# Performance work log

Measured on AMD Instinct MI355X. Metric: run time of the kernel, lower is better.

Reference implementation:

```python
import jax, jax.numpy as jnp
import numpy as np

B, LT, D, H, DI = 8, 128, 512, 8, 2048
NMEM, LMEM = 1024, 64
DH = D // H
EPS = 1e-5
NEG = -1e9

def _ln(x, g, b):
    mu = x.mean(-1, keepdims=True)
    var = ((x - mu) ** 2).mean(-1, keepdims=True)
    return (x - mu) * jax.lax.rsqrt(var + EPS) * g + b

def _ffn(x, W1, b1, W2, b2):
    # PositionwiseFF with residual=True (dropout=0 / eval)
    return x + jax.nn.relu(x @ W1 + b1) @ W2 + b2

def setup_inputs():
    key = jax.random.key(0)
    ks = jax.random.split(key, 16)
    w = lambda i, shape: jax.random.normal(ks[i], shape, jnp.float32) * 0.02
    return {
        "dec_output": jax.random.normal(ks[0], (B, LT, D), jnp.float32),
        "mem_attn_out": jax.random.normal(ks[1], (B, LT, NMEM + 1), jnp.float32),
        "enc_out_mem": jax.random.normal(ks[2], (NMEM, LMEM, D), jnp.float32),
        "tgt_emb_mem": jax.random.normal(ks[3], (NMEM, LMEM, D), jnp.float32),
        "tgt_mask_mem": jax.random.randint(ks[4], (NMEM, LMEM), 0, 2, jnp.int32),
        "tgt_mask": jax.random.randint(ks[5], (B, LT), 0, 2, jnp.int32),
        "g0": jnp.ones((D,), jnp.float32), "be0": jnp.zeros((D,), jnp.float32),
        "g1": jnp.ones((D,), jnp.float32), "be1": jnp.zeros((D,), jnp.float32),
        "Wq": w(6, (D, D)), "bq": jnp.zeros((D,), jnp.float32),
        "Wk": w(7, (D, D)), "bk": jnp.zeros((D,), jnp.float32),
        "Wv": w(8, (D, D)), "bv": jnp.zeros((D,), jnp.float32),
        "Wo": w(9, (D, D)), "bo": jnp.zeros((D,), jnp.float32),
        "f1W1": w(10, (D, DI)), "f1b1": jnp.zeros((DI,), jnp.float32),
        "f1W2": w(11, (DI, D)), "f1b2": jnp.zeros((D,), jnp.float32),
        "f2W1": w(12, (D, DI)), "f2b1": jnp.zeros((DI,), jnp.float32),
        "f2W2": w(13, (DI, D)), "f2b2": jnp.zeros((D,), jnp.float32),
    }

def reference(dec_output, mem_attn_out, enc_out_mem, tgt_emb_mem, tgt_mask_mem, tgt_mask,
              g0, be0, g1, be1, Wq, bq, Wk, bk, Wv, bv, Wo, bo,
              f1W1, f1b1, f1W2, f1b2, f2W1, f2b1, f2W2, f2b2):
    x = _ln(dec_output, g0, be0)                       # [B,LT,D]
    N = B * LT
    samples = jnp.argmax(mem_attn_out, -1).reshape(N) - 1   # [-1, NMEM-1]
    valid = samples >= 0                               # [N]
    s = jnp.maximum(samples, 0)                        # clamp; masked later
    q = x.reshape(N, 1, D)
    # gather memory per selected query (torch compacts via unique; same math)
    k_in = enc_out_mem[s]                              # [N,LMEM,D]
    v_in = tgt_emb_mem[s]                              # [N,LMEM,D]
    kmask = tgt_mask_mem[s] != 0                       # True = valid key
    # multi-head attention, residual=True
    qh = (q @ Wq + bq).reshape(N, 1, H, DH).transpose(0, 2, 1, 3)     # [N,H,1,DH]
    kh = (k_in @ Wk + bk).reshape(N, LMEM, H, DH).transpose(0, 2, 1, 3)
    vh = (v_in @ Wv + bv).reshape(N, LMEM, H, DH).transpose(0, 2, 1, 3)
    scores = jnp.einsum('nhqd,nhkd->nhqk', qh, kh) / (DH ** 0.5)      # [N,H,1,LMEM]
    scores = jnp.where(kmask[:, None, None, :], scores, NEG)
    attn = jax.nn.softmax(scores, axis=-1)
    ctx = jnp.einsum('nhqk,nhkd->nhqd', attn, vh).transpose(0, 2, 1, 3).reshape(N, 1, D)
    st = q + ctx @ Wo + bo
    st = _ffn(st, f1W1, f1b1, f1W2, f1b2)
    st = _ln(st, g1, be1)
    # scatter back: positions with sample == -1 get zeros
    st = jnp.where(valid[:, None, None], st, 0.0)
    dec = x + st.reshape(B, LT, D)
    dec = _ffn(dec, f2W1, f2b1, f2W2, f2b2)
    return dec
```

## Files before the change

kernel.cpp:

```cpp
#include <hip/hip_runtime.h>
#include <math.h>

#define NQ   1024
#define DIM  512
#define NH   8
#define DHD  64
#define DFF  2048
#define LM   64

typedef __bf16 bf16x8 __attribute__((ext_vector_type(8)));
typedef float  f32x4  __attribute__((ext_vector_type(4)));

__device__ __forceinline__ unsigned short f2bf(float f) {
    unsigned u = __builtin_bit_cast(unsigned, f);
    return (unsigned short)((u + 0x7fffu + ((u >> 16) & 1u)) >> 16);
}
__device__ __forceinline__ float bflo(unsigned p) {
    return __builtin_bit_cast(float, p << 16);
}
__device__ __forceinline__ float bfhi(unsigned p) {
    return __builtin_bit_cast(float, p & 0xffff0000u);
}

__device__ __forceinline__ void gload16(const void* g, void* l) {
    __builtin_amdgcn_global_load_lds(
        (const __attribute__((address_space(1))) unsigned*)g,
        (__attribute__((address_space(3))) unsigned*)l, 16, 0, 0);
}

__device__ __forceinline__ float blk_sum(float v, volatile float* red) {
#pragma unroll
    for (int o = 32; o; o >>= 1) v += __shfl_down(v, o);
    __syncthreads();
    if ((threadIdx.x & 63) == 0) red[threadIdx.x >> 6] = v;
    __syncthreads();
    return red[0] + red[1] + red[2] + red[3];
}

struct PrepPtrs {
    const float* src[8];
    unsigned short* dst[8];
};
__global__ __launch_bounds__(256) void prep_ln0_k(
    PrepPtrs p,
    const float* __restrict__ dec_out, const float* __restrict__ attn_out,
    const float* __restrict__ g, const float* __restrict__ be,
    float* __restrict__ x, unsigned* __restrict__ xb, int* __restrict__ samples)
{
    __shared__ float tile[32][33];
    __shared__ float red[4];
    __shared__ float rv[4]; __shared__ int ri[4];
    const int bid = blockIdx.x;

    if (bid < 5120) {
        int m, lt;
        if (bid < 1024) { m = bid >> 8; lt = bid & 255; }
        else { m = 4 + ((bid - 1024) >> 10); lt = (bid - 1024) & 1023; }
        const int RS = (m < 4) ? 512 : ((m == 5 || m == 7) ? 2048 : 512);
        const int CS = (m < 4) ? 512 : ((m == 5 || m == 7) ? 512 : 2048);
        const int TC = CS >> 5;
        const int tr = lt / TC, tc = lt % TC;
        const float* s = p.src[m];
        unsigned short* d = p.dst[m];
        const int tx = threadIdx.x & 31, ty = threadIdx.x >> 5;
        if (m == 1) {
#pragma unroll
            for (int i = 0; i < 32; i += 8) {
                size_t idx = (size_t)(tr * 32 + ty + i) * CS + tc * 32 + tx;
                d[idx] = f2bf(s[idx]);
            }
        } else {
#pragma unroll
            for (int i = 0; i < 32; i += 8)
                tile[ty + i][tx] = s[(size_t)(tr * 32 + ty + i) * CS + tc * 32 + tx];
            __syncthreads();
#pragma unroll
            for (int i = 0; i < 32; i += 8)
                d[(size_t)(tc * 32 + ty + i) * RS + tr * 32 + tx] = f2bf(tile[tx][ty + i]);
        }
        return;
    }

    const int n = bid - 5120, t = threadIdx.x;
    float2 v = ((const float2*)(dec_out + (size_t)n * DIM))[t];
    float mu  = blk_sum(v.x + v.y, red) * (1.f / DIM);
    float dx = v.x - mu, dy = v.y - mu;
    float var = blk_sum(dx * dx + dy * dy, red) * (1.f / DIM);
    float rs = rsqrtf(var + 1e-5f);
    float2 gg = ((const float2*)g)[t], bb = ((const float2*)be)[t];
    float ox = dx * rs * gg.x + bb.x, oy = dy * rs * gg.y + bb.y;
    ((float2*)(x + (size_t)n * DIM))[t] = make_float2(ox, oy);
    xb[(size_t)n * 256 + t] = (unsigned)f2bf(ox) | ((unsigned)f2bf(oy) << 16);

    const float* ar = attn_out + (size_t)n * 1025;
    float bv = -INFINITY; int bi = 0x7fffffff;
    for (int i = t; i < 1025; i += 256) {
        float val = ar[i];
        if (val > bv || (val == bv && i < bi)) { bv = val; bi = i; }
    }
#pragma unroll
    for (int o = 32; o; o >>= 1) {
        float ov = __shfl_down(bv, o); int oi = __shfl_down(bi, o);
        if (ov > bv || (ov == bv && oi < bi)) { bv = ov; bi = oi; }
    }
    if ((t & 63) == 0) { rv[t >> 6] = bv; ri[t >> 6] = bi; }
    __syncthreads();
    if (t == 0) {
#pragma unroll
        for (int w = 1; w < 4; ++w)
            if (rv[w] > bv || (rv[w] == bv && ri[w] < bi)) { bv = rv[w]; bi = ri[w]; }
        samples[n] = bi - 1;
    }
}

template<bool RELU, bool BIAS, bool RES, bool WF32, bool WBF>
__global__ __launch_bounds__(256) void mfma_gemm(
    const unsigned short* __restrict__ A, const unsigned short* __restrict__ Bt,
    float* __restrict__ Cf, unsigned short* __restrict__ Cb,
    const float* __restrict__ bias, const float* __restrict__ res,
    int K, int lda, int ldb, int ldc,
    int sA, int sB, int sC, int sBias)
{
    __shared__ unsigned short Ab[2][64 * 64];
    __shared__ unsigned short Bb[2][64 * 64];
    const int t = threadIdx.x, lane = t & 63, wid = t >> 6;
    const int nx = gridDim.x;
    const int fid = blockIdx.y * nx + blockIdx.x;
    const int cpx = (nx * gridDim.y) >> 3;
    const int f2 = (fid & 7) * cpx + (fid >> 3);
    const int bn = (f2 % nx) * 64, bm = (f2 / nx) * 64, bz = blockIdx.z;
    const unsigned short* Abase = A + (size_t)bz * sA + (size_t)bm * lda;
    const unsigned short* Bbase = Bt + (size_t)bz * sB + (size_t)bn * ldb;

    const int r0 = wid * 16 + (lane >> 3);
    const int cbs = lane & 7;

#define STAGE_T(buf, base, ld, kt)                                              \
    {                                                                           \
        int r_ = r0;                                                            \
        gload16(base + (size_t)r_ * ld + (kt) * 64 + ((cbs ^ (r_ & 7)) << 3),   \
                &buf[(wid * 2 + 0) * 512]);                                     \
        r_ = r0 + 8;                                                            \
        gload16(base + (size_t)r_ * ld + (kt) * 64 + ((cbs ^ (r_ & 7)) << 3),   \
                &buf[(wid * 2 + 1) * 512]);                                     \
    }

    const int lr = lane & 15, lg = lane >> 4;
    const int wr = (wid >> 1) * 32, wc = (wid & 1) * 32;
    const int mA0 = wr + lr, mA1 = wr + 16 + lr;
    const int nB0 = wc + lr, nB1 = wc + 16 + lr;
    f32x4 acc[2][2] = {};

#define COMPUTE(b)                                                              \
    _Pragma("unroll")                                                           \
    for (int kk = 0; kk < 2; ++kk) {                                            \
        const int kb = kk * 4 + lg;                                             \
        bf16x8 a0 = *(const bf16x8*)&Ab[b][mA0 * 64 + ((kb ^ (mA0 & 7)) << 3)]; \
        bf16x8 a1 = *(const bf16x8*)&Ab[b][mA1 * 64 + ((kb ^ (mA1 & 7)) << 3)]; \
        bf16x8 b0 = *(const bf16x8*)&Bb[b][nB0 * 64 + ((kb ^ (nB0 & 7)) << 3)]; \
        bf16x8 b1 = *(const bf16x8*)&Bb[b][nB1 * 64 + ((kb ^ (nB1 & 7)) << 3)]; \
        acc[0][0] = __builtin_amdgcn_mfma_f32_16x16x32_bf16(a0, b0, acc[0][0], 0, 0, 0); \
        acc[0][1] = __builtin_amdgcn_mfma_f32_16x16x32_bf16(a0, b1, acc[0][1], 0, 0, 0); \
        acc[1][0] = __builtin_amdgcn_mfma_f32_16x16x32_bf16(a1, b0, acc[1][0], 0, 0, 0); \
        acc[1][1] = __builtin_amdgcn_mfma_f32_16x16x32_bf16(a1, b1, acc[1][1], 0, 0, 0); \
    }

    STAGE_T(Ab[0], Abase, lda, 0);
    STAGE_T(Bb[0], Bbase, ldb, 0);
    __syncthreads();
    const int NT = K >> 6;
    int cur = 0;
    for (int kt = 0; kt < NT; ++kt) {
        if (kt + 1 < NT) {
            STAGE_T(Ab[cur ^ 1], Abase, lda, kt + 1);
            STAGE_T(Bb[cur ^ 1], Bbase, ldb, kt + 1);
        }
        if (cur == 0) { COMPUTE(0); } else { COMPUTE(1); }
        __syncthreads();
        cur ^= 1;
    }

#pragma unroll
    for (int fm = 0; fm < 2; ++fm)
#pragma unroll
    for (int fn = 0; fn < 2; ++fn) {
        const int col = bn + wc + fn * 16 + lr;
        float bia = BIAS ? bias[bz * sBias + col] : 0.f;
#pragma unroll
        for (int r = 0; r < 4; ++r) {
            const int row = bm + wr + fm * 16 + lg * 4 + r;
            const size_t ci = (size_t)bz * sC + (size_t)row * ldc + col;
            float v = acc[fm][fn][r] + bia;
            if (RES) v += res[(size_t)row * ldc + col];
            if (RELU) v = fmaxf(v, 0.f);
            if (WF32) Cf[ci] = v;
            if (WBF)  Cb[ci] = f2bf(v);
        }
    }
#undef STAGE_T
#undef COMPUTE
}

__global__ __launch_bounds__(256) void attn_scores_k(
    const unsigned short* __restrict__ u_bf, const float* __restrict__ enc,
    const int* __restrict__ samples, float* __restrict__ s_part)
{
    const int n = blockIdx.x, q = blockIdx.y, t = threadIdx.x;
    const int lane = t & 63, w = t >> 6;
    int s = samples[n]; if (s < 0) s = 0;

    const float4* kb = (const float4*)(enc + (size_t)s * (LM * DIM));
    const int key = w * 16 + (lane & 15);
    const int lg = lane >> 4;
    const int h = lane & 15;
    const int base = key * 128 + q * 32 + lg * 2;
    float4 pf[4][2];
#pragma unroll
    for (int ss = 0; ss < 4; ++ss) {
        pf[ss][0] = kb[base + ss * 8];
        pf[ss][1] = kb[base + ss * 8 + 1];
    }

    const unsigned short* ub = u_bf + (size_t)n * 4096 + (size_t)(h & 7) * 512 + q * 128;
    f32x4 acc = {};
#pragma unroll
    for (int step = 0; step < 4; ++step) {
        float4 a0 = pf[step][0], a1 = pf[step][1];
        bf16x8 af;
        af[0] = (__bf16)a0.x; af[1] = (__bf16)a0.y;
        af[2] = (__bf16)a0.z; af[3] = (__bf16)a0.w;
        af[4] = (__bf16)a1.x; af[5] = (__bf16)a1.y;
        af[6] = (__bf16)a1.z; af[7] = (__bf16)a1.w;
        bf16x8 bfr = *(const bf16x8*)&ub[(step * 4 + lg) * 8];
        acc = __builtin_amdgcn_mfma_f32_16x16x32_bf16(af, bfr, acc, 0, 0, 0);
    }
    if (h < 8) {
        float* sp = s_part + (((size_t)n * 4 + q) * 8 + h) * 64 + w * 16 + lg * 4;
        *(float4*)sp = make_float4(acc[0], acc[1], acc[2], acc[3]);
    }
}

__global__ __launch_bounds__(256) void attn_pv_k(
    const float* __restrict__ s_part, const float* __restrict__ vemb,
    const int* __restrict__ maskmem, const int* __restrict__ samples,
    unsigned* __restrict__ a_bf)
{
    __shared__ float Sp_lds[2048];
    __shared__ uint4 P_lds[64];
    __shared__ float2 Red[3][8][64];
    __shared__ int Msk_lds[64];
    const int n = blockIdx.x, dq = blockIdx.y, t = threadIdx.x;
    const int lane = t & 63, w = t >> 6;
    int s = samples[n]; if (s < 0) s = 0;

    ((float4*)Sp_lds)[t]       = ((const float4*)(s_part + (size_t)n * 2048))[t];
    ((float4*)Sp_lds)[t + 256] = ((const float4*)(s_part + (size_t)n * 2048))[t + 256];
    if (t < 64) Msk_lds[t] = maskmem[(size_t)s * LM + t];
    __syncthreads();

#pragma unroll
    for (int hh = 0; hh < 2; ++hh) {
        const int h = w + hh * 4;
        float sc = (Sp_lds[h * 64 + lane] + Sp_lds[512 + h * 64 + lane]
                  + Sp_lds[1024 + h * 64 + lane] + Sp_lds[1536 + h * 64 + lane]) * 0.125f;
        sc = (Msk_lds[lane] != 0) ? sc : -1e9f;
        float m = sc;
#pragma unroll
        for (int o = 32; o; o >>= 1) m = fmaxf(m, __shfl_xor(m, o));
        float e = __expf(sc - m);
        float su = e;
#pragma unroll
        for (int o = 32; o; o >>= 1) su += __shfl_xor(su, o);
        ((unsigned short*)P_lds)[lane * 8 + h] = f2bf(e / su);
    }
    __syncthreads();

    const int c = t & 63, kh = t >> 6;
    const float2* vb = (const float2*)(vemb + (size_t)s * (LM * DIM)) + dq * 64 + c;
    float2 acc8[8];
#pragma unroll
    for (int hh = 0; hh < 8; ++hh) acc8[hh] = make_float2(0.f, 0.f);
#pragma unroll 8
    for (int i = 0; i < 16; ++i) {
        const int k = kh * 16 + i;
        float2 v = vb[(size_t)k * 256];
        uint4 pr = P_lds[k];
        float p0 = bflo(pr.x), p1 = bfhi(pr.x);
        float p2 = bflo(pr.y), p3 = bfhi(pr.y);
        float p4 = bflo(pr.z), p5 = bfhi(pr.z);
        float p6 = bflo(pr.w), p7 = bfhi(pr.w);
        acc8[0].x = fmaf(p0, v.x, acc8[0].x); acc8[0].y = fmaf(p0, v.y, acc8[0].y);
        acc8[1].x = fmaf(p1, v.x, acc8[1].x); acc8[1].y = fmaf(p1, v.y, acc8[1].y);
        acc8[2].x = fmaf(p2, v.x, acc8[2].x); acc8[2].y = fmaf(p2, v.y, acc8[2].y);
        acc8[3].x = fmaf(p3, v.x, acc8[3].x); acc8[3].y = fmaf(p3, v.y, acc8[3].y);
        acc8[4].x = fmaf(p4, v.x, acc8[4].x); acc8[4].y = fmaf(p4, v.y, acc8[4].y);
        acc8[5].x = fmaf(p5, v.x, acc8[5].x); acc8[5].y = fmaf(p5, v.y, acc8[5].y);
        acc8[6].x = fmaf(p6, v.x, acc8[6].x); acc8[6].y = fmaf(p6, v.y, acc8[6].y);
        acc8[7].x = fmaf(p7, v.x, acc8[7].x); acc8[7].y = fmaf(p7, v.y, acc8[7].y);
    }
    if (kh > 0) {
#pragma unroll
        for (int hh = 0; hh < 8; ++hh) Red[kh - 1][hh][c] = acc8[hh];
    }
    __syncthreads();
    if (kh == 0) {
        unsigned* an = a_bf + (size_t)n * 2048 + dq * 64;
#pragma unroll
        for (int hh = 0; hh < 8; ++hh) {
            float2 r0 = Red[0][hh][c], r1 = Red[1][hh][c], r2 = Red[2][hh][c];
            float ox = acc8[hh].x + r0.x + r1.x + r2.x;
            float oy = acc8[hh].y + r0.y + r1.y + r2.y;
            an[hh * 256 + c] = (unsigned)f2bf(ox) | ((unsigned)f2bf(oy) << 16);
        }
    }
}

__global__ __launch_bounds__(256) void ln1_mask_add_k(
    const float* __restrict__ t1p, const float* __restrict__ st0,
    const float* __restrict__ b2, const float* __restrict__ g,
    const float* __restrict__ be, const int* __restrict__ samples,
    const float* __restrict__ x, float* __restrict__ dec, unsigned* __restrict__ decb)
{
    __shared__ float red[4];
    const int n = blockIdx.x, t = threadIdx.x;
    const size_t off = (size_t)n * DIM + t * 2;
    float2 p0 = *(const float2*)&t1p[off];
    float2 p1 = *(const float2*)&t1p[(size_t)NQ * DIM + off];
    float2 s0 = *(const float2*)&st0[off];
    float2 b2v = ((const float2*)b2)[t];
    float2 v = make_float2(p0.x + p1.x + s0.x + b2v.x, p0.y + p1.y + s0.y + b2v.y);
    float mu  = blk_sum(v.x + v.y, red) * (1.f / DIM);
    float dx = v.x - mu, dy = v.y - mu;
    float var = blk_sum(dx * dx + dy * dy, red) * (1.f / DIM);
    float rs = rsqrtf(var + 1e-5f);
    float2 gg = ((const float2*)g)[t], bb = ((const float2*)be)[t];
    float sx = dx * rs * gg.x + bb.x, sy = dy * rs * gg.y + bb.y;
    if (samples[n] < 0) { sx = 0.f; sy = 0.f; }
    float2 xx = *(const float2*)&x[off];
    float ox = xx.x + sx, oy = xx.y + sy;
    *(float2*)&dec[off] = make_float2(ox, oy);
    decb[(size_t)n * 256 + t] = (unsigned)f2bf(ox) | ((unsigned)f2bf(oy) << 16);
}

extern "C" void kernel_launch(void* const* d_in, const int* in_sizes, int n_in,
                              void* d_out, int out_size, void* d_ws, size_t ws_size,
                              hipStream_t stream)
{
    const float* dec_output = (const float*)d_in[0];
    const float* mem_attn   = (const float*)d_in[1];
    const float* enc_mem    = (const float*)d_in[2];
    const float* temb_mem   = (const float*)d_in[3];
    const int*   mask_mem   = (const int*)d_in[4];
    const float* g0  = (const float*)d_in[6];
    const float* be0 = (const float*)d_in[7];
    const float* g1  = (const float*)d_in[8];
    const float* be1 = (const float*)d_in[9];
    const float* Wq  = (const float*)d_in[10];
    const float* bq  = (const float*)d_in[11];
    const float* Wk  = (const float*)d_in[12];
    const float* Wv  = (const float*)d_in[14];
    const float* bv  = (const float*)d_in[15];
    const float* Wo  = (const float*)d_in[16];
    const float* bo  = (const float*)d_in[17];
    const float* f1W1 = (const float*)d_in[18];
    const float* f1b1 = (const float*)d_in[19];
    const float* f1W2 = (const float*)d_in[20];
    const float* f1b2 = (const float*)d_in[21];
    const float* f2W1 = (const float*)d_in[22];
    const float* f2b1 = (const float*)d_in[23];
    const float* f2W2 = (const float*)d_in[24];
    const float* f2b2 = (const float*)d_in[25];
    float* out = (float*)d_out;

    float* ws = (float*)d_ws;
    float*          x_f   = ws + 0;
    unsigned*       x_b   = (unsigned*)(ws + 524288);
    unsigned short* qh_b  = (unsigned short*)(ws + 786432);
    unsigned short* u_b   = (unsigned short*)(ws + 1048576);
    unsigned short* a_b   = (unsigned short*)(ws + 3145728);
    float*          s_prt = ws + 5242880;
    unsigned short* wqt   = (unsigned short*)(ws + 7340032);
    unsigned short* wkc   = (unsigned short*)(ws + 7471104);
    unsigned short* wvt   = (unsigned short*)(ws + 7602176);
    unsigned short* wot   = (unsigned short*)(ws + 7733248);
    unsigned short* f1w1t = (unsigned short*)(ws + 7864320);
    unsigned short* f1w2t = (unsigned short*)(ws + 8388608);
    unsigned short* f2w1t = (unsigned short*)(ws + 8912896);
    unsigned short* f2w2t = (unsigned short*)(ws + 9437184);
    int*            smp   = (int*)(ws + 9961472);
    float*          t1p_f = ws + 9962496;
    float*          st0_f = (float*)u_b + 0;
    unsigned short* st0_b = (unsigned short*)((float*)u_b + 524288);
    float*          dec_f = (float*)u_b + 655360;
    unsigned*       dec_b = (unsigned*)((float*)u_b + 1179648);
    unsigned short* h1_b  = a_b;
    unsigned short* h2_b  = (unsigned short*)((float*)a_b + 1048576);

    PrepPtrs pp;
    pp.src[0] = Wq;   pp.dst[0] = wqt;
    pp.src[1] = Wk;   pp.dst[1] = wkc;
    pp.src[2] = Wv;   pp.dst[2] = wvt;
    pp.src[3] = Wo;   pp.dst[3] = wot;
    pp.src[4] = f1W1; pp.dst[4] = f1w1t;
    pp.src[5] = f1W2; pp.dst[5] = f1w2t;
    pp.src[6] = f2W1; pp.dst[6] = f2w1t;
    pp.src[7] = f2W2; pp.dst[7] = f2w2t;
    prep_ln0_k<<<5120 + NQ, 256, 0, stream>>>(pp, dec_output, mem_attn, g0, be0,
                                              x_f, x_b, smp);
    mfma_gemm<false, true, false, false, true><<<dim3(8, 16, 1), 256, 0, stream>>>(
        (const unsigned short*)x_b, wqt, nullptr, qh_b, bq, nullptr,
        DIM, DIM, DIM, DIM, 0, 0, 0, 0);
    mfma_gemm<false, false, false, false, true><<<dim3(8, 16, NH), 256, 0, stream>>>(
        qh_b, wkc, nullptr, u_b, nullptr, nullptr,
        DHD, DIM, DIM, NH * DIM, DHD, DHD, DIM, 0);
    attn_scores_k<<<dim3(NQ, 4), 256, 0, stream>>>(u_b, enc_mem, smp, s_prt);
    attn_pv_k<<<dim3(NQ, 4), 256, 0, stream>>>(s_prt, temb_mem, mask_mem, smp,
                                               (unsigned*)a_b);
    mfma_gemm<false, true, false, false, true><<<dim3(1, 16, NH), 256, 0, stream>>>(
        a_b, wvt, nullptr, qh_b, bv, nullptr,
        DIM, NH * DIM, DIM, DIM, DIM, DHD * DIM, DHD, DHD);
    mfma_gemm<false, true, true, true, true><<<dim3(8, 16, 1), 256, 0, stream>>>(
        qh_b, wot, st0_f, st0_b, bo, x_f, DIM, DIM, DIM, DIM, 0, 0, 0, 0);
    mfma_gemm<true, true, false, false, true><<<dim3(32, 16, 1), 256, 0, stream>>>(
        st0_b, f1w1t, nullptr, h1_b, f1b1, nullptr, DIM, DIM, DIM, DFF, 0, 0, 0, 0);
    mfma_gemm<false, false, false, true, false><<<dim3(8, 16, 2), 256, 0, stream>>>(
        h1_b, f1w2t, t1p_f, nullptr, nullptr, nullptr,
        1024, DFF, DFF, DIM, 1024, 1024, NQ * DIM, 0);
    ln1_mask_add_k<<<NQ, 256, 0, stream>>>(t1p_f, st0_f, f1b2, g1, be1, smp,
                                           x_f, dec_f, dec_b);
    mfma_gemm<true, true, false, false, true><<<dim3(32, 16, 1), 256, 0, stream>>>(
        (const unsigned short*)dec_b, f2w1t, nullptr, h2_b, f2b1, nullptr,
        DIM, DIM, DIM, DFF, 0, 0, 0, 0);
    mfma_gemm<false, true, true, true, false><<<dim3(8, 16, 1), 256, 0, stream>>>(
        h2_b, f2w2t, out, nullptr, f2b2, dec_f, DFF, DFF, DFF, DIM, 0, 0, 0, 0);

    (void)in_sizes; (void)n_in; (void)out_size; (void)ws_size;
}
```

Before: 156.7 us.

## Fuse partial softmax into score kernel and split keys across blocks

The score kernel now splits work by key halves instead of D-quarters. Each block reduces the full 512-dim dot product in-block through LDS, applies the mask, and computes a local softmax (max, sum, unnormalized bf16 exp). The PV kernel then merges the two halves with flash-style rescaling instead of re-reading 2048 float partial scores per query and redoing the softmax. The change also software-pipelines the K loads, reorders the PV grid so the four D-quarter blocks of one query are adjacent, and cuts intermediate traffic. The cost is an extra bf16 rounding of the rescaled probabilities and fewer, heavier score blocks.

Result: faster. 153.2 us (-2.2%).

```diff
diff --git a/kernel.cpp b/kernel.cpp
--- a/kernel.cpp
+++ b/kernel.cpp
@@ -203,29 +203,36 @@
 
 __global__ __launch_bounds__(256) void attn_scores_k(
     const unsigned short* __restrict__ u_bf, const float* __restrict__ enc,
-    const int* __restrict__ samples, float* __restrict__ s_part)
-{
-    const int n = blockIdx.x, q = blockIdx.y, t = threadIdx.x;
+    const int* __restrict__ maskmem, const int* __restrict__ samples,
+    unsigned short* __restrict__ p_half, float* __restrict__ msc)
+{
+    __shared__ float S_lds[2][32][8];
+    const int n = blockIdx.x, kq = blockIdx.y, t = threadIdx.x;
     const int lane = t & 63, w = t >> 6;
     int s = samples[n]; if (s < 0) s = 0;
 
-    const float4* kb = (const float4*)(enc + (size_t)s * (LM * DIM));
-    const int key = w * 16 + (lane & 15);
+    const int keyloc = (w & 1) * 16 + (lane & 15);
+    const int key = kq * 32 + keyloc;
+    const int dh = w >> 1;
     const int lg = lane >> 4;
     const int h = lane & 15;
-    const int base = key * 128 + q * 32 + lg * 2;
+    const float4* kb = (const float4*)(enc + (size_t)s * (LM * DIM));
+    const int base = key * 128 + dh * 64 + lg * 2;
     float4 pf[4][2];
 #pragma unroll
     for (int ss = 0; ss < 4; ++ss) {
         pf[ss][0] = kb[base + ss * 8];
         pf[ss][1] = kb[base + ss * 8 + 1];
     }
-
-    const unsigned short* ub = u_bf + (size_t)n * 4096 + (size_t)(h & 7) * 512 + q * 128;
+    const unsigned short* ub = u_bf + (size_t)n * 4096 + (size_t)(h & 7) * 512 + dh * 256;
     f32x4 acc = {};
 #pragma unroll
-    for (int step = 0; step < 4; ++step) {
-        float4 a0 = pf[step][0], a1 = pf[step][1];
+    for (int step = 0; step < 8; ++step) {
+        float4 a0 = pf[step & 3][0], a1 = pf[step & 3][1];
+        if (step + 4 < 8) {
+            pf[step & 3][0] = kb[base + (step + 4) * 8];
+            pf[step & 3][1] = kb[base + (step + 4) * 8 + 1];
+        }
         bf16x8 af;
         af[0] = (__bf16)a0.x; af[1] = (__bf16)a0.y;
         af[2] = (__bf16)a0.z; af[3] = (__bf16)a0.w;
@@ -235,43 +242,54 @@
         acc = __builtin_amdgcn_mfma_f32_16x16x32_bf16(af, bfr, acc, 0, 0, 0);
     }
     if (h < 8) {
-        float* sp = s_part + (((size_t)n * 4 + q) * 8 + h) * 64 + w * 16 + lg * 4;
-        *(float4*)sp = make_float4(acc[0], acc[1], acc[2], acc[3]);
-    }
+#pragma unroll
+        for (int r = 0; r < 4; ++r)
+            S_lds[dh][(w & 1) * 16 + lg * 4 + r][h] = acc[r];
+    }
+    __syncthreads();
+
+    const int h2 = t >> 5, k2 = t & 31;
+    float sc = (S_lds[0][k2][h2] + S_lds[1][k2][h2]) * 0.125f;
+    const int mk = maskmem[(size_t)s * LM + kq * 32 + k2];
+    sc = (mk != 0) ? sc : -1e9f;
+    float m = sc;
+#pragma unroll
+    for (int o = 16; o; o >>= 1) m = fmaxf(m, __shfl_xor(m, o));
+    float e = __expf(sc - m);
+    float su = e;
+#pragma unroll
+    for (int o = 16; o; o >>= 1) su += __shfl_xor(su, o);
+    p_half[((size_t)n * 2 + kq) * 256 + k2 * 8 + h2] = f2bf(e);
+    if (k2 == 0)
+        ((float2*)(msc + ((size_t)n * 2 + kq) * 16))[h2] = make_float2(m, su);
 }
 
 __global__ __launch_bounds__(256) void attn_pv_k(
-    const float* __restrict__ s_part, const float* __restrict__ vemb,
-    const int* __restrict__ maskmem, const int* __restrict__ samples,
+    const unsigned short* __restrict__ p_half, const float* __restrict__ msc,
+    const float* __restrict__ vemb, const int* __restrict__ samples,
     unsigned* __restrict__ a_bf)
 {
-    __shared__ float Sp_lds[2048];
     __shared__ uint4 P_lds[64];
     __shared__ float2 Red[3][8][64];
-    __shared__ int Msk_lds[64];
-    const int n = blockIdx.x, dq = blockIdx.y, t = threadIdx.x;
-    const int lane = t & 63, w = t >> 6;
+    __shared__ float Wh[2][8];
+    const int dq = blockIdx.x, n = blockIdx.y, t = threadIdx.x;
     int s = samples[n]; if (s < 0) s = 0;
 
-    ((float4*)Sp_lds)[t]       = ((const float4*)(s_part + (size_t)n * 2048))[t];
-    ((float4*)Sp_lds)[t + 256] = ((const float4*)(s_part + (size_t)n * 2048))[t + 256];
-    if (t < 64) Msk_lds[t] = maskmem[(size_t)s * LM + t];
-    __syncthreads();
-
-#pragma unroll
-    for (int hh = 0; hh < 2; ++hh) {
-        const int h = w + hh * 4;
-        float sc = (Sp_lds[h * 64 + lane] + Sp_lds[512 + h * 64 + lane]
-                  + Sp_lds[1024 + h * 64 + lane] + Sp_lds[1536 + h * 64 + lane]) * 0.125f;
-        sc = (Msk_lds[lane] != 0) ? sc : -1e9f;
-        float m = sc;
-#pragma unroll
-        for (int o = 32; o; o >>= 1) m = fmaxf(m, __shfl_xor(m, o));
-        float e = __expf(sc - m);
-        float su = e;
-#pragma unroll
-        for (int o = 32; o; o >>= 1) su += __shfl_xor(su, o);
-        ((unsigned short*)P_lds)[lane * 8 + h] = f2bf(e / su);
+    if (t < 8) {
+        float2 ms0 = ((const float2*)(msc + (size_t)n * 32))[t];
+        float2 ms1 = ((const float2*)(msc + (size_t)n * 32 + 16))[t];
+        float m = fmaxf(ms0.x, ms1.x);
+        float w0 = __expf(ms0.x - m), w1 = __expf(ms1.x - m);
+        float inv = 1.f / (ms0.y * w0 + ms1.y * w1);
+        Wh[0][t] = w0 * inv; Wh[1][t] = w1 * inv;
+    }
+    __syncthreads();
+    {
+        const int k = t >> 2, hp = t & 3, kq = k >> 5;
+        unsigned v = ((const unsigned*)p_half)[((size_t)n * 2 + kq) * 128 + (k & 31) * 4 + hp];
+        float a = bflo(v) * Wh[kq][hp * 2];
+        float b = bfhi(v) * Wh[kq][hp * 2 + 1];
+        ((unsigned*)P_lds)[k * 4 + hp] = (unsigned)f2bf(a) | ((unsigned)f2bf(b) << 16);
     }
     __syncthreads();
 
@@ -378,7 +396,8 @@
     unsigned short* qh_b  = (unsigned short*)(ws + 786432);
     unsigned short* u_b   = (unsigned short*)(ws + 1048576);
     unsigned short* a_b   = (unsigned short*)(ws + 3145728);
-    float*          s_prt = ws + 5242880;
+    unsigned short* p_hlf = (unsigned short*)(ws + 5242880);
+    float*          msc   = ws + 5505024;
     unsigned short* wqt   = (unsigned short*)(ws + 7340032);
     unsigned short* wkc   = (unsigned short*)(ws + 7471104);
     unsigned short* wvt   = (unsigned short*)(ws + 7602176);
@@ -413,8 +432,9 @@
     mfma_gemm<false, false, false, false, true><<<dim3(8, 16, NH), 256, 0, stream>>>(
         qh_b, wkc, nullptr, u_b, nullptr, nullptr,
         DHD, DIM, DIM, NH * DIM, DHD, DHD, DIM, 0);
-    attn_scores_k<<<dim3(NQ, 4), 256, 0, stream>>>(u_b, enc_mem, smp, s_prt);
-    attn_pv_k<<<dim3(NQ, 4), 256, 0, stream>>>(s_prt, temb_mem, mask_mem, smp,
+    attn_scores_k<<<dim3(NQ, 2), 256, 0, stream>>>(u_b, enc_mem, mask_mem, smp,
+                                                   p_hlf, msc);
+    attn_pv_k<<<dim3(4, NQ), 256, 0, stream>>>(p_hlf, msc, temb_mem, smp,
                                                (unsigned*)a_b);
     mfma_gemm<false, true, false, false, true><<<dim3(1, 16, NH), 256, 0, stream>>>(
         a_b, wvt, nullptr, qh_b, bv, nullptr,
```

## Fuse attention scores, softmax and PV into one warp-specialized kernel

Applied to the files above, without the earlier changes.

Merges the separate score and PV kernels into one 512-thread block per query. Four waves compute the full QK scores over all of D with register-prefetched MFMA, while the other four waves prefetch V rows in parallel, then do the whole 64-key PV loop themselves. This drops the global score-partial round trip, one launch, and the cross-wave LDS reduction. The cost is fewer, larger blocks and longer serial loops per thread, which may reduce parallelism and occupancy.

New measurement: 149.9 us. 1.05x faster.

```diff
diff --git a/kernel.cpp b/kernel.cpp
--- a/kernel.cpp
+++ b/kernel.cpp
@@ -201,117 +201,106 @@
 #undef COMPUTE
 }
 
-__global__ __launch_bounds__(256) void attn_scores_k(
+__global__ __launch_bounds__(512) void attn_fused_k(
     const unsigned short* __restrict__ u_bf, const float* __restrict__ enc,
-    const int* __restrict__ samples, float* __restrict__ s_part)
+    const float* __restrict__ vemb, const int* __restrict__ maskmem,
+    const int* __restrict__ samples, unsigned* __restrict__ a_bf)
 {
-    const int n = blockIdx.x, q = blockIdx.y, t = threadIdx.x;
+    __shared__ float S_lds[8 * 68];
+    __shared__ uint4 P_lds[64];
+    __shared__ int Msk_lds[64];
+    const int n = blockIdx.x, t = threadIdx.x;
     const int lane = t & 63, w = t >> 6;
     int s = samples[n]; if (s < 0) s = 0;
 
-    const float4* kb = (const float4*)(enc + (size_t)s * (LM * DIM));
-    const int key = w * 16 + (lane & 15);
-    const int lg = lane >> 4;
-    const int h = lane & 15;
-    const int base = key * 128 + q * 32 + lg * 2;
-    float4 pf[4][2];
-#pragma unroll
-    for (int ss = 0; ss < 4; ++ss) {
-        pf[ss][0] = kb[base + ss * 8];
-        pf[ss][1] = kb[base + ss * 8 + 1];
-    }
-
-    const unsigned short* ub = u_bf + (size_t)n * 4096 + (size_t)(h & 7) * 512 + q * 128;
-    f32x4 acc = {};
-#pragma unroll
-    for (int step = 0; step < 4; ++step) {
-        float4 a0 = pf[step][0], a1 = pf[step][1];
-        bf16x8 af;
-        af[0] = (__bf16)a0.x; af[1] = (__bf16)a0.y;
-        af[2] = (__bf16)a0.z; af[3] = (__bf16)a0.w;
-        af[4] = (__bf16)a1.x; af[5] = (__bf16)a1.y;
-        af[6] = (__bf16)a1.z; af[7] = (__bf16)a1.w;
-        bf16x8 bfr = *(const bf16x8*)&ub[(step * 4 + lg) * 8];
-        acc = __builtin_amdgcn_mfma_f32_16x16x32_bf16(af, bfr, acc, 0, 0, 0);
-    }
-    if (h < 8) {
-        float* sp = s_part + (((size_t)n * 4 + q) * 8 + h) * 64 + w * 16 + lg * 4;
-        *(float4*)sp = make_float4(acc[0], acc[1], acc[2], acc[3]);
-    }
-}
-
-__global__ __launch_bounds__(256) void attn_pv_k(
-    const float* __restrict__ s_part, const float* __restrict__ vemb,
-    const int* __restrict__ maskmem, const int* __restrict__ samples,
-    unsigned* __restrict__ a_bf)
-{
-    __shared__ float Sp_lds[2048];
-    __shared__ uint4 P_lds[64];
-    __shared__ float2 Red[3][8][64];
-    __shared__ int Msk_lds[64];
-    const int n = blockIdx.x, dq = blockIdx.y, t = threadIdx.x;
-    const int lane = t & 63, w = t >> 6;
-    int s = samples[n]; if (s < 0) s = 0;
-
-    ((float4*)Sp_lds)[t]       = ((const float4*)(s_part + (size_t)n * 2048))[t];
-    ((float4*)Sp_lds)[t + 256] = ((const float4*)(s_part + (size_t)n * 2048))[t + 256];
-    if (t < 64) Msk_lds[t] = maskmem[(size_t)s * LM + t];
-    __syncthreads();
-
-#pragma unroll
-    for (int hh = 0; hh < 2; ++hh) {
-        const int h = w + hh * 4;
-        float sc = (Sp_lds[h * 64 + lane] + Sp_lds[512 + h * 64 + lane]
-                  + Sp_lds[1024 + h * 64 + lane] + Sp_lds[1536 + h * 64 + lane]) * 0.125f;
-        sc = (Msk_lds[lane] != 0) ? sc : -1e9f;
-        float m = sc;
-#pragma unroll
-        for (int o = 32; o; o >>= 1) m = fmaxf(m, __shfl_xor(m, o));
-        float e = __expf(sc - m);
-        float su = e;
-#pragma unroll
-        for (int o = 32; o; o >>= 1) su += __shfl_xor(su, o);
-        ((unsigned short*)P_lds)[lane * 8 + h] = f2bf(e / su);
-    }
-    __syncthreads();
-
-    const int c = t & 63, kh = t >> 6;
-    const float2* vb = (const float2*)(vemb + (size_t)s * (LM * DIM)) + dq * 64 + c;
-    float2 acc8[8];
-#pragma unroll
-    for (int hh = 0; hh < 8; ++hh) acc8[hh] = make_float2(0.f, 0.f);
+    float2 pfv[8];
+    const float2* vb = (const float2*)(vemb + (size_t)s * (LM * DIM)) + (t - 256);
+
+    if (w >= 4) {
+#pragma unroll
+        for (int i = 0; i < 8; ++i) pfv[i] = vb[(size_t)i * 256];
+        if (w == 4) Msk_lds[lane] = maskmem[(size_t)s * LM + lane];
+    } else {
+        const float4* kb = (const float4*)(enc + (size_t)s * (LM * DIM));
+        const int key = w * 16 + (lane & 15);
+        const int lg = lane >> 4;
+        const int h = lane & 15;
+        const int base = key * 128 + lg * 2;
+        float4 pf[4][2];
+#pragma unroll
+        for (int ss = 0; ss < 4; ++ss) {
+            pf[ss][0] = kb[base + ss * 8];
+            pf[ss][1] = kb[base + ss * 8 + 1];
+        }
+        const unsigned short* ub = u_bf + (size_t)n * 4096 + (size_t)(h & 7) * 512;
+        f32x4 acc = {};
+#pragma unroll
+        for (int step = 0; step < 16; ++step) {
+            float4 a0 = pf[step & 3][0], a1 = pf[step & 3][1];
+            if (step + 4 < 16) {
+                pf[step & 3][0] = kb[base + (step + 4) * 8];
+                pf[step & 3][1] = kb[base + (step + 4) * 8 + 1];
+            }
+            bf16x8 af;
+            af[0] = (__bf16)a0.x; af[1] = (__bf16)a0.y;
+            af[2] = (__bf16)a0.z; af[3] = (__bf16)a0.w;
+            af[4] = (__bf16)a1.x; af[5] = (__bf16)a1.y;
+            af[6] = (__bf16)a1.z; af[7] = (__bf16)a1.w;
+            bf16x8 bfr = *(const bf16x8*)&ub[(step * 4 + lg) * 8];
+            acc = __builtin_amdgcn_mfma_f32_16x16x32_bf16(af, bfr, acc, 0, 0, 0);
+        }
+        if (h < 8) {
+#pragma unroll
+            for (int r = 0; r < 4; ++r)
+                S_lds[h * 68 + w * 16 + lg * 4 + r] = acc[r];
+        }
+    }
+    __syncthreads();
+
+    if (w < 4) {
+#pragma unroll
+        for (int hh = 0; hh < 2; ++hh) {
+            const int h2 = w + hh * 4;
+            float sc = S_lds[h2 * 68 + lane] * 0.125f;
+            sc = (Msk_lds[lane] != 0) ? sc : -1e9f;
+            float m = sc;
+#pragma unroll
+            for (int o = 32; o; o >>= 1) m = fmaxf(m, __shfl_xor(m, o));
+            float e = __expf(sc - m);
+            float su = e;
+#pragma unroll
+            for (int o = 32; o; o >>= 1) su += __shfl_xor(su, o);
+            ((unsigned short*)P_lds)[lane * 8 + h2] = f2bf(e / su);
+        }
+    }
+    __syncthreads();
+
+    if (w >= 4) {
+        float2 acc8[8];
+#pragma unroll
+        for (int hh = 0; hh < 8; ++hh) acc8[hh] = make_float2(0.f, 0.f);
 #pragma unroll 8
-    for (int i = 0; i < 16; ++i) {
-        const int k = kh * 16 + i;
-        float2 v = vb[(size_t)k * 256];
-        uint4 pr = P_lds[k];
-        float p0 = bflo(pr.x), p1 = bfhi(pr.x);
-        float p2 = bflo(pr.y), p3 = bfhi(pr.y);
-        float p4 = bflo(pr.z), p5 = bfhi(pr.z);
-        float p6 = bflo(pr.w), p7 = bfhi(pr.w);
-        acc8[0].x = fmaf(p0, v.x, acc8[0].x); acc8[0].y = fmaf(p0, v.y, acc8[0].y);
-        acc8[1].x = fmaf(p1, v.x, acc8[1].x); acc8[1].y = fmaf(p1, v.y, acc8[1].y);
-        acc8[2].x = fmaf(p2, v.x, acc8[2].x); acc8[2].y = fmaf(p2, v.y, acc8[2].y);
-        acc8[3].x = fmaf(p3, v.x, acc8[3].x); acc8[3].y = fmaf(p3, v.y, acc8[3].y);
-        acc8[4].x = fmaf(p4, v.x, acc8[4].x); acc8[4].y = fmaf(p4, v.y, acc8[4].y);
-        acc8[5].x = fmaf(p5, v.x, acc8[5].x); acc8[5].y = fmaf(p5, v.y, acc8[5].y);
-        acc8[6].x = fmaf(p6, v.x, acc8[6].x); acc8[6].y = fmaf(p6, v.y, acc8[6].y);
-        acc8[7].x = fmaf(p7, v.x, acc8[7].x); acc8[7].y = fmaf(p7, v.y, acc8[7].y);
-    }
-    if (kh > 0) {
-#pragma unroll
-        for (int hh = 0; hh < 8; ++hh) Red[kh - 1][hh][c] = acc8[hh];
-    }
-    __syncthreads();
-    if (kh == 0) {
-        unsigned* an = a_bf + (size_t)n * 2048 + dq * 64;
-#pragma unroll
-        for (int hh = 0; hh < 8; ++hh) {
-            float2 r0 = Red[0][hh][c], r1 = Red[1][hh][c], r2 = Red[2][hh][c];
-            float ox = acc8[hh].x + r0.x + r1.x + r2.x;
-            float oy = acc8[hh].y + r0.y + r1.y + r2.y;
-            an[hh * 256 + c] = (unsigned)f2bf(ox) | ((unsigned)f2bf(oy) << 16);
-        }
+        for (int k = 0; k < 64; ++k) {
+            float2 v = pfv[k & 7];
+            if (k + 8 < 64) pfv[k & 7] = vb[(size_t)(k + 8) * 256];
+            uint4 pr = P_lds[k];
+            float p0 = bflo(pr.x), p1 = bfhi(pr.x);
+            float p2 = bflo(pr.y), p3 = bfhi(pr.y);
+            float p4 = bflo(pr.z), p5 = bfhi(pr.z);
+            float p6 = bflo(pr.w), p7 = bfhi(pr.w);
+            acc8[0].x = fmaf(p0, v.x, acc8[0].x); acc8[0].y = fmaf(p0, v.y, acc8[0].y);
+            acc8[1].x = fmaf(p1, v.x, acc8[1].x); acc8[1].y = fmaf(p1, v.y, acc8[1].y);
+            acc8[2].x = fmaf(p2, v.x, acc8[2].x); acc8[2].y = fmaf(p2, v.y, acc8[2].y);
+            acc8[3].x = fmaf(p3, v.x, acc8[3].x); acc8[3].y = fmaf(p3, v.y, acc8[3].y);
+            acc8[4].x = fmaf(p4, v.x, acc8[4].x); acc8[4].y = fmaf(p4, v.y, acc8[4].y);
+            acc8[5].x = fmaf(p5, v.x, acc8[5].x); acc8[5].y = fmaf(p5, v.y, acc8[5].y);
+            acc8[6].x = fmaf(p6, v.x, acc8[6].x); acc8[6].y = fmaf(p6, v.y, acc8[6].y);
+            acc8[7].x = fmaf(p7, v.x, acc8[7].x); acc8[7].y = fmaf(p7, v.y, acc8[7].y);
+        }
+        unsigned* an = a_bf + (size_t)n * 2048 + (t - 256);
+#pragma unroll
+        for (int hh = 0; hh < 8; ++hh)
+            an[hh * 256] = (unsigned)f2bf(acc8[hh].x) | ((unsigned)f2bf(acc8[hh].y) << 16);
     }
 }
 
@@ -378,7 +367,6 @@
     unsigned short* qh_b  = (unsigned short*)(ws + 786432);
     unsigned short* u_b   = (unsigned short*)(ws + 1048576);
     unsigned short* a_b   = (unsigned short*)(ws + 3145728);
-    float*          s_prt = ws + 5242880;
     unsigned short* wqt   = (unsigned short*)(ws + 7340032);
     unsigned short* wkc   = (unsigned short*)(ws + 7471104);
     unsigned short* wvt   = (unsigned short*)(ws + 7602176);
@@ -413,9 +401,8 @@
     mfma_gemm<false, false, false, false, true><<<dim3(8, 16, NH), 256, 0, stream>>>(
         qh_b, wkc, nullptr, u_b, nullptr, nullptr,
         DHD, DIM, DIM, NH * DIM, DHD, DHD, DIM, 0);
-    attn_scores_k<<<dim3(NQ, 4), 256, 0, stream>>>(u_b, enc_mem, smp, s_prt);
-    attn_pv_k<<<dim3(NQ, 4), 256, 0, stream>>>(s_prt, temb_mem, mask_mem, smp,
-                                               (unsigned*)a_b);
+    attn_fused_k<<<NQ, 512, 0, stream>>>(u_b, enc_mem, temb_mem, mask_mem, smp,
+                                         (unsigned*)a_b);
     mfma_gemm<false, true, false, false, true><<<dim3(1, 16, NH), 256, 0, stream>>>(
         a_b, wvt, nullptr, qh_b, bv, nullptr,
         DIM, NH * DIM, DIM, DIM, DIM, DHD * DIM, DHD, DHD);
```
